# Kernel tuning notes

Hardware: AMD Instinct MI355X
Metric: run time of the kernel (lower is better)

The kernel has to match this reference:

```python
import jax, jax.numpy as jnp
import numpy as np

FACTOR = 5

def setup_inputs() -> dict:
    key = jax.random.key(0)
    kq, kk, kv, ki = jax.random.split(key, 4)
    B, L, H, D = 4, 4096, 8, 64
    sample_k = min(int(FACTOR * np.ceil(np.log(L))), L)  # 45
    queries = jax.random.normal(kq, (B, L, H, D), dtype=jnp.float32)
    keys = jax.random.normal(kk, (B, L, H, D), dtype=jnp.float32)
    values = jax.random.normal(kv, (B, L, H, D), dtype=jnp.float32)
    index_sample = jax.random.randint(ki, (L, sample_k), 0, L, dtype=jnp.int64)
    return {"queries": queries, "keys": keys, "values": values, "index_sample": index_sample}


def reference(queries, keys, values, index_sample):
    # queries/keys/values: (B, L, H, D); mask_flag=False, output_attention=False
    B, L_Q, H, D = queries.shape
    L_K = keys.shape[1]
    n_top = min(int(FACTOR * np.ceil(np.log(L_Q))), L_Q)
    scale = 1.0 / np.sqrt(D)

    Q = jnp.transpose(queries, (0, 2, 1, 3))  # (B,H,L_Q,D)
    K = jnp.transpose(keys, (0, 2, 1, 3))     # (B,H,L_K,D)
    V = jnp.transpose(values, (0, 2, 1, 3))   # (B,H,L_V,D)

    # --- _prob_QK: sample keys per query, score sparsity, keep top queries ---
    K_sample = K[:, :, index_sample, :]                       # (B,H,L_Q,S,D)
    Q_K_sample = jnp.einsum('bhqd,bhqsd->bhqs', Q, K_sample)  # (B,H,L_Q,S)
    M = Q_K_sample.max(axis=-1) - Q_K_sample.mean(axis=-1)    # (B,H,L_Q)
    _, M_top = jax.lax.top_k(M, n_top)                        # (B,H,n_top)
    Q_reduce = jnp.take_along_axis(Q, M_top[..., None], axis=2)  # (B,H,n_top,D)
    scores = jnp.einsum('bhnd,bhkd->bhnk', Q_reduce, K) * scale # (B,H,n_top,L_K)

    # --- initial context (mask_flag=False): mean of V over keys ---
    context = jnp.broadcast_to(V.mean(axis=2, keepdims=True), (B, H, L_Q, D))

    # --- update context at selected query positions ---
    attn = jax.nn.softmax(scores, axis=-1)                    # (B,H,n_top,L_K)
    upd = jnp.einsum('bhnk,bhkd->bhnd', attn, V)              # (B,H,n_top,D)
    bi = jnp.arange(B)[:, None, None]
    hi = jnp.arange(H)[None, :, None]
    context = context.at[bi, hi, M_top].set(upd)
    return context
```

## Files before the change

### kernel.cpp

```cpp
#include <hip/hip_runtime.h>
#include <math.h>

#define B_   4
#define L_   4096
#define H_   8
#define D_   64
#define SK   45
#define NT   45
#define BH   (B_*H_)
#define SCALE 0.125f
#define KC   256
#define JC2  16
#define VCH  64

typedef float vfloat4 __attribute__((ext_vector_type(4)));

__global__ __launch_bounds__(256) void k_m(const float* __restrict__ q,
                                           const float* __restrict__ k,
                                           const int* __restrict__ samp,
                                           float* __restrict__ M) {
  __shared__ int sid[8 * SK];
  const int ib   = blockIdx.x;
  const int x    = ib & 7;
  const int b    = x >> 1;
  const int half = x & 1;
  const int qi_base = (ib >> 3) * 8;
  const int tid = threadIdx.x;
  for (int i = tid; i < 8 * SK; i += 256)
    sid[i] = samp[(size_t)qi_base * SK + i];
  __syncthreads();

  const int w    = tid >> 6;
  const int lane = tid & 63;
  const int g2   = lane >> 5;
  const int l32  = lane & 31;
  const int hg   = l32 >> 3;
  const int r8   = l32 & 7;
  const int qi   = qi_base + w * 2 + g2;
  const int wq   = w * 2 + g2;

  const float* qbase = q + (((size_t)b * L_ + qi) * H_ + half * 4 + hg) * D_ + r8 * 8;
  const vfloat4 qa = __builtin_nontemporal_load((const vfloat4*)qbase);
  const vfloat4 qb4 = __builtin_nontemporal_load((const vfloat4*)(qbase + 4));

  const int* myids = sid + wq * SK;
  const float* kb2 = k + (size_t)b * L_ * (H_ * D_) + (half * 4 + hg) * D_ + r8 * 8;

  float gmax = -1e30f, gsum = 0.f;
  #pragma unroll 5
  for (int s = 0; s < SK; ++s) {
    const int id = myids[s];
    const float* kr = kb2 + (size_t)id * (H_ * D_);
    const vfloat4 ka  = *(const vfloat4*)kr;
    const vfloat4 kbv = *(const vfloat4*)(kr + 4);
    float p = qa.x*ka.x + qa.y*ka.y + qa.z*ka.z + qa.w*ka.w
            + qb4.x*kbv.x + qb4.y*kbv.y + qb4.z*kbv.z + qb4.w*kbv.w;
    { int t = __builtin_amdgcn_mov_dpp(__float_as_int(p), 0xB1, 0xf, 0xf, true); p += __int_as_float(t); }
    { int t = __builtin_amdgcn_mov_dpp(__float_as_int(p), 0x4E, 0xf, 0xf, true); p += __int_as_float(t); }
    { int t = __builtin_amdgcn_mov_dpp(__float_as_int(p), 0x141, 0xf, 0xf, true); p += __int_as_float(t); }
    gmax = fmaxf(gmax, p);
    gsum += p;
  }
  if (r8 == 0) M[((size_t)b * 8 + half * 4 + hg) * L_ + qi] = gmax - gsum * (1.0f / SK);
}

__global__ __launch_bounds__(256) void k_topk(const float* __restrict__ M,
                                              int* __restrict__ top) {
  __shared__ unsigned keys[L_];
  __shared__ unsigned hist[256];
  __shared__ unsigned wsum[4];
  __shared__ int sByte;
  __shared__ unsigned sAbove;
  __shared__ int cnt;
  const int bh = blockIdx.x, tid = threadIdx.x;
  const float* Mrow = M + (size_t)bh * L_;
  for (int i = tid; i < L_; i += 256) {
    const unsigned u = __float_as_uint(Mrow[i]);
    keys[i] = (u & 0x80000000u) ? ~u : (u | 0x80000000u);
  }
  unsigned prefix = 0u, fixed = 0u;
  unsigned remaining = NT;
  for (int p = 3; p >= 0; --p) {
    hist[tid] = 0u;
    __syncthreads();
    const int sh = p * 8;
    for (int i = tid; i < L_; i += 256) {
      const unsigned kk = keys[i];
      if ((kk & fixed) == prefix) atomicAdd(&hist[(kk >> sh) & 0xFFu], 1u);
    }
    __syncthreads();
    const int c = 255 - tid;
    const unsigned v = hist[c];
    unsigned x = v;
    #pragma unroll
    for (int o = 1; o < 64; o <<= 1) {
      const unsigned y = __shfl_up(x, o);
      if ((tid & 63) >= o) x += y;
    }
    if ((tid & 63) == 63) wsum[tid >> 6] = x;
    __syncthreads();
    unsigned off = 0;
    for (int w2 = 0; w2 < (tid >> 6); ++w2) off += wsum[w2];
    const unsigned Sincl = x + off;
    const unsigned Sab   = Sincl - v;
    if (Sab < remaining && remaining <= Sincl) { sByte = c; sAbove = Sab; }
    __syncthreads();
    prefix |= (unsigned)sByte << sh;
    fixed  |= 0xFFu << sh;
    remaining -= sAbove;
    __syncthreads();
  }
  if (tid == 0) cnt = 0;
  __syncthreads();
  int* trow = top + bh * NT;
  for (int i = tid; i < L_; i += 256) {
    if (keys[i] > prefix) { const int s = atomicAdd(&cnt, 1); trow[s] = i; }
  }
  __syncthreads();
  const int ngt = cnt;
  const int base = tid * 16;
  int lc = 0;
  #pragma unroll
  for (int j = 0; j < 16; ++j) lc += (keys[base + j] == prefix);
  unsigned x2 = (unsigned)lc;
  #pragma unroll
  for (int o = 1; o < 64; o <<= 1) {
    const unsigned y = __shfl_up(x2, o);
    if ((tid & 63) >= o) x2 += y;
  }
  if ((tid & 63) == 63) wsum[tid >> 6] = x2;
  __syncthreads();
  unsigned off2 = 0;
  for (int w2 = 0; w2 < (tid >> 6); ++w2) off2 += wsum[w2];
  unsigned rk = (x2 - (unsigned)lc) + off2;
  #pragma unroll
  for (int j = 0; j < 16; ++j) {
    if (keys[base + j] == prefix) {
      if (rk < remaining) trow[ngt + (int)rk] = base + j;
      ++rk;
    }
  }
}

__global__ __launch_bounds__(256) void k_vmean1(const float* __restrict__ v,
                                                float* __restrict__ vpart) {
  const int blk = blockIdx.x;
  const int b   = blk >> 6;
  const int c   = blk & 63;
  const int t   = threadIdx.x;
  const int hd4 = t & 127;
  const int p   = t >> 7;
  const float4* base = (const float4*)(v + ((size_t)b * L_ + (size_t)c * VCH) * (H_ * D_)) + hd4;
  float4 acc = {0.f, 0.f, 0.f, 0.f};
  for (int l = p; l < VCH; l += 2) {
    const float4 x = base[(size_t)l * 128];
    acc.x += x.x; acc.y += x.y; acc.z += x.z; acc.w += x.w;
  }
  __shared__ float4 s[2][128];
  s[p][hd4] = acc;
  __syncthreads();
  if (t < 128) {
    const float4 a = s[0][t], b2 = s[1][t];
    const float4 r = {a.x + b2.x, a.y + b2.y, a.z + b2.z, a.w + b2.w};
    ((float4*)vpart)[(size_t)blk * 128 + t] = r;
  }
}

__global__ __launch_bounds__(512) void k_vmean2(const float* __restrict__ vpart,
                                                float* __restrict__ vmean) {
  const int b = blockIdx.x, t = threadIdx.x;
  float acc = 0.f;
  for (int c = 0; c < 64; ++c)
    acc += vpart[((size_t)(b * 64 + c)) * 512 + t];
  vmean[b * 512 + t] = acc * (1.0f / L_);
}

__global__ __launch_bounds__(512) void k_attn(const float* __restrict__ q,
                                              const float* __restrict__ k,
                                              const float* __restrict__ v,
                                              const int* __restrict__ top,
                                              float* __restrict__ ml,
                                              float* __restrict__ opart) {
  __shared__ float lds_p[NT * 260];
  __shared__ __align__(16) float lds_q[NT * 64];
  __shared__ float lds_ml[NT * 2];
  const int bh = blockIdx.x >> 4, jc = blockIdx.x & 15;
  const int b = bh >> 3, h = bh & 7;
  const int tid = threadIdx.x;

  for (int fi = tid; fi < NT * 64; fi += 512) {
    const int n = fi >> 6, d = fi & 63;
    const int qi = top[bh * NT + n];
    lds_q[fi] = q[(((size_t)b * L_ + qi) * H_ + h) * D_ + d];
  }
  __syncthreads();

  {
    const int j = tid >> 1, dh = tid & 1;
    const float* krow_g = k + (((size_t)b * L_ + jc * KC + j) * H_ + h) * D_ + dh * 32;
    float kr[32];
    #pragma unroll
    for (int t4 = 0; t4 < 8; ++t4) {
      const vfloat4 kv = *(const vfloat4*)(krow_g + t4 * 4);
      kr[t4*4+0] = kv.x; kr[t4*4+1] = kv.y; kr[t4*4+2] = kv.z; kr[t4*4+3] = kv.w;
    }
    for (int n = 0; n < NT; ++n) {
      const float* qrow = &lds_q[n * 64 + dh * 32];
      float s = 0.f;
      #pragma unroll
      for (int t4 = 0; t4 < 8; ++t4) {
        const float4 qq = *(const float4*)(qrow + t4 * 4);
        s += qq.x*kr[t4*4] + qq.y*kr[t4*4+1] + qq.z*kr[t4*4+2] + qq.w*kr[t4*4+3];
      }
      { int t = __builtin_amdgcn_mov_dpp(__float_as_int(s), 0xB1, 0xf, 0xf, true); s += __int_as_float(t); }
      if (dh == 0) lds_p[n * 260 + j] = s * SCALE;
    }
  }
  __syncthreads();

  const int w = tid >> 6, lane = tid & 63;
  for (int n = w; n < NT; n += 8) {
    float* pr = &lds_p[n * 260];
    const float s0 = pr[lane], s1 = pr[64 + lane], s2 = pr[128 + lane], s3 = pr[192 + lane];
    float m = fmaxf(fmaxf(s0, s1), fmaxf(s2, s3));
    #pragma unroll
    for (int o = 1; o < 64; o <<= 1) m = fmaxf(m, __shfl_xor(m, o));
    const float p0 = __expf(s0 - m), p1 = __expf(s1 - m), p2 = __expf(s2 - m), p3 = __expf(s3 - m);
    float lsum = p0 + p1 + p2 + p3;
    #pragma unroll
    for (int o = 1; o < 64; o <<= 1) lsum += __shfl_xor(lsum, o);
    pr[lane] = p0; pr[64 + lane] = p1; pr[128 + lane] = p2; pr[192 + lane] = p3;
    if (lane == 0) { lds_ml[n * 2] = m; lds_ml[n * 2 + 1] = lsum; }
  }
  __syncthreads();

  const int d = lane;
  const int nn = (w < 5) ? 6 : 5;
  float acc[6];
  #pragma unroll
  for (int t = 0; t < 6; ++t) acc[t] = 0.f;
  const float* vbase = v + (((size_t)b * L_ + jc * KC) * H_ + h) * D_ + d;
  for (int j4 = 0; j4 < KC; j4 += 4) {
    float vv[4];
    #pragma unroll
    for (int u = 0; u < 4; ++u) vv[u] = vbase[(size_t)(j4 + u) * (H_ * D_)];
    #pragma unroll
    for (int t = 0; t < 6; ++t) {
      if (t < nn) {
        const int n = w + 8 * t;
        const float4 pv = *(const float4*)&lds_p[n * 260 + j4];
        acc[t] += pv.x * vv[0] + pv.y * vv[1] + pv.z * vv[2] + pv.w * vv[3];
      }
    }
  }
  float* obase = opart + (((size_t)bh * JC2 + jc) * NT) * 64;
  #pragma unroll
  for (int t = 0; t < 6; ++t)
    if (t < nn) obase[(w + 8 * t) * 64 + d] = acc[t];
  for (int i = tid; i < NT * 2; i += 512)
    ml[((size_t)bh * JC2 + jc) * (NT * 2) + i] = lds_ml[i];
}

__global__ __launch_bounds__(256) void k_fill(const float* __restrict__ vmean,
                                              float* __restrict__ out) {
  const size_t i = (size_t)blockIdx.x * 256 + threadIdx.x;
  const int d4 = (int)(i & 15);
  const int bh = (int)(i >> 16);
  const float4* vm = (const float4*)(vmean + bh * D_);
  ((float4*)out)[i] = vm[d4];
}

__global__ void k_comb(const float* __restrict__ opart,
                       const float* __restrict__ ml,
                       const int* __restrict__ top,
                       float* __restrict__ out) {
  const int bhn = blockIdx.x, bh = bhn / NT, n = bhn % NT;
  const int d = threadIdx.x;
  float mc[JC2], lc[JC2];
  float mg = -1e30f;
  #pragma unroll
  for (int c = 0; c < JC2; ++c) {
    mc[c] = ml[((size_t)bh * JC2 + c) * (NT * 2) + n * 2];
    lc[c] = ml[((size_t)bh * JC2 + c) * (NT * 2) + n * 2 + 1];
    mg = fmaxf(mg, mc[c]);
  }
  float den = 0.f, num = 0.f;
  #pragma unroll
  for (int c = 0; c < JC2; ++c) {
    const float wgt = __expf(mc[c] - mg);
    den += wgt * lc[c];
    num += wgt * opart[(((size_t)bh * JC2 + c) * NT + n) * 64 + d];
  }
  const int qi = top[bh * NT + n];
  out[((size_t)bh * L_ + qi) * 64 + d] = num / den;
}

extern "C" void kernel_launch(void* const* d_in, const int* in_sizes, int n_in,
                              void* d_out, int out_size, void* d_ws, size_t ws_size,
                              hipStream_t stream) {
  const float* q    = (const float*)d_in[0];
  const float* k    = (const float*)d_in[1];
  const float* v    = (const float*)d_in[2];
  const int*   samp = (const int*)d_in[3];
  float* out = (float*)d_out;
  char*  ws  = (char*)d_ws;

  float* M     = (float*)ws;
  int*   top   = (int*)(ws + 524288);
  float* vmean = (float*)(ws + 532480);
  float* opart = (float*)(ws + 540672);
  float* vpart = M;
  float* ml    = M;

  hipLaunchKernelGGL(k_m,      dim3(BH * L_ / 32), dim3(256), 0, stream, q, k, samp, M);
  hipLaunchKernelGGL(k_topk,   dim3(BH),           dim3(256), 0, stream, M, top);
  hipLaunchKernelGGL(k_vmean1, dim3(B_ * 64),      dim3(256), 0, stream, v, vpart);
  hipLaunchKernelGGL(k_vmean2, dim3(B_),           dim3(512), 0, stream, vpart, vmean);
  hipLaunchKernelGGL(k_attn,   dim3(BH * JC2),     dim3(512), 0, stream, q, k, v, top, ml, opart);
  hipLaunchKernelGGL(k_fill,   dim3(8192),         dim3(256), 0, stream, vmean, out);
  hipLaunchKernelGGL(k_comb,   dim3(BH * NT),      dim3(64),  0, stream, opart, ml, top, out);
}
```

Baseline: 156.6 us.

## Merge independent kernels via block-index dispatch and raise wave priority in attention loops

Merges seven launches into four by giving independent jobs their own block ranges. M-scoring runs alongside the V partial sums, top-k alongside the V-mean reduction, and attention alongside the mean fill of the output. This cuts launch gaps and lets small kernels share the GPU. The V partials move into the opart workspace so they do not clash with M. It also wraps the QK and PV loops in s_setprio to favour compute waves, at the cost of larger merged kernels whose LDS and register budget is set by the heaviest branch.

```diff
diff --git a/kernel.cpp b/kernel.cpp
--- a/kernel.cpp
+++ b/kernel.cpp
@@ -15,64 +15,101 @@
 
 typedef float vfloat4 __attribute__((ext_vector_type(4)));
 
-__global__ __launch_bounds__(256) void k_m(const float* __restrict__ q,
-                                           const float* __restrict__ k,
-                                           const int* __restrict__ samp,
-                                           float* __restrict__ M) {
-  __shared__ int sid[8 * SK];
-  const int ib   = blockIdx.x;
-  const int x    = ib & 7;
-  const int b    = x >> 1;
-  const int half = x & 1;
-  const int qi_base = (ib >> 3) * 8;
+__global__ __launch_bounds__(256) void k_mv(const float* __restrict__ q,
+                                            const float* __restrict__ k,
+                                            const int* __restrict__ samp,
+                                            const float* __restrict__ v,
+                                            float* __restrict__ M,
+                                            float* __restrict__ vpart) {
   const int tid = threadIdx.x;
-  for (int i = tid; i < 8 * SK; i += 256)
-    sid[i] = samp[(size_t)qi_base * SK + i];
-  __syncthreads();
-
-  const int w    = tid >> 6;
-  const int lane = tid & 63;
-  const int g2   = lane >> 5;
-  const int l32  = lane & 31;
-  const int hg   = l32 >> 3;
-  const int r8   = l32 & 7;
-  const int qi   = qi_base + w * 2 + g2;
-  const int wq   = w * 2 + g2;
-
-  const float* qbase = q + (((size_t)b * L_ + qi) * H_ + half * 4 + hg) * D_ + r8 * 8;
-  const vfloat4 qa = __builtin_nontemporal_load((const vfloat4*)qbase);
-  const vfloat4 qb4 = __builtin_nontemporal_load((const vfloat4*)(qbase + 4));
-
-  const int* myids = sid + wq * SK;
-  const float* kb2 = k + (size_t)b * L_ * (H_ * D_) + (half * 4 + hg) * D_ + r8 * 8;
-
-  float gmax = -1e30f, gsum = 0.f;
-  #pragma unroll 5
-  for (int s = 0; s < SK; ++s) {
-    const int id = myids[s];
-    const float* kr = kb2 + (size_t)id * (H_ * D_);
-    const vfloat4 ka  = *(const vfloat4*)kr;
-    const vfloat4 kbv = *(const vfloat4*)(kr + 4);
-    float p = qa.x*ka.x + qa.y*ka.y + qa.z*ka.z + qa.w*ka.w
-            + qb4.x*kbv.x + qb4.y*kbv.y + qb4.z*kbv.z + qb4.w*kbv.w;
-    { int t = __builtin_amdgcn_mov_dpp(__float_as_int(p), 0xB1, 0xf, 0xf, true); p += __int_as_float(t); }
-    { int t = __builtin_amdgcn_mov_dpp(__float_as_int(p), 0x4E, 0xf, 0xf, true); p += __int_as_float(t); }
-    { int t = __builtin_amdgcn_mov_dpp(__float_as_int(p), 0x141, 0xf, 0xf, true); p += __int_as_float(t); }
-    gmax = fmaxf(gmax, p);
-    gsum += p;
-  }
-  if (r8 == 0) M[((size_t)b * 8 + half * 4 + hg) * L_ + qi] = gmax - gsum * (1.0f / SK);
-}
-
-__global__ __launch_bounds__(256) void k_topk(const float* __restrict__ M,
-                                              int* __restrict__ top) {
+  if (blockIdx.x < 4096) {
+    __shared__ int sid[8 * SK];
+    const int ib   = blockIdx.x;
+    const int x    = ib & 7;
+    const int b    = x >> 1;
+    const int half = x & 1;
+    const int qi_base = (ib >> 3) * 8;
+    for (int i = tid; i < 8 * SK; i += 256)
+      sid[i] = samp[(size_t)qi_base * SK + i];
+    __syncthreads();
+
+    const int w    = tid >> 6;
+    const int lane = tid & 63;
+    const int g2   = lane >> 5;
+    const int l32  = lane & 31;
+    const int hg   = l32 >> 3;
+    const int r8   = l32 & 7;
+    const int qi   = qi_base + w * 2 + g2;
+    const int wq   = w * 2 + g2;
+
+    const float* qbase = q + (((size_t)b * L_ + qi) * H_ + half * 4 + hg) * D_ + r8 * 8;
+    const vfloat4 qa = __builtin_nontemporal_load((const vfloat4*)qbase);
+    const vfloat4 qb4 = __builtin_nontemporal_load((const vfloat4*)(qbase + 4));
+
+    const int* myids = sid + wq * SK;
+    const float* kb2 = k + (size_t)b * L_ * (H_ * D_) + (half * 4 + hg) * D_ + r8 * 8;
+
+    float gmax = -1e30f, gsum = 0.f;
+    #pragma unroll 5
+    for (int s = 0; s < SK; ++s) {
+      const int id = myids[s];
+      const float* kr = kb2 + (size_t)id * (H_ * D_);
+      const vfloat4 ka  = *(const vfloat4*)kr;
+      const vfloat4 kbv = *(const vfloat4*)(kr + 4);
+      float p = qa.x*ka.x + qa.y*ka.y + qa.z*ka.z + qa.w*ka.w
+              + qb4.x*kbv.x + qb4.y*kbv.y + qb4.z*kbv.z + qb4.w*kbv.w;
+      { int t = __builtin_amdgcn_mov_dpp(__float_as_int(p), 0xB1, 0xf, 0xf, true); p += __int_as_float(t); }
+      { int t = __builtin_amdgcn_mov_dpp(__float_as_int(p), 0x4E, 0xf, 0xf, true); p += __int_as_float(t); }
+      { int t = __builtin_amdgcn_mov_dpp(__float_as_int(p), 0x141, 0xf, 0xf, true); p += __int_as_float(t); }
+      gmax = fmaxf(gmax, p);
+      gsum += p;
+    }
+    if (r8 == 0) M[((size_t)b * 8 + half * 4 + hg) * L_ + qi] = gmax - gsum * (1.0f / SK);
+  } else {
+    const int blk = blockIdx.x - 4096;
+    const int b   = blk >> 6;
+    const int c   = blk & 63;
+    const int hd4 = tid & 127;
+    const int p   = tid >> 7;
+    const float4* base = (const float4*)(v + ((size_t)b * L_ + (size_t)c * VCH) * (H_ * D_)) + hd4;
+    float4 acc = {0.f, 0.f, 0.f, 0.f};
+    for (int l = p; l < VCH; l += 2) {
+      const float4 xv = base[(size_t)l * 128];
+      acc.x += xv.x; acc.y += xv.y; acc.z += xv.z; acc.w += xv.w;
+    }
+    __shared__ float4 s[2][128];
+    s[p][hd4] = acc;
+    __syncthreads();
+    if (tid < 128) {
+      const float4 a = s[0][tid], b2 = s[1][tid];
+      const float4 r = {a.x + b2.x, a.y + b2.y, a.z + b2.z, a.w + b2.w};
+      ((float4*)vpart)[(size_t)blk * 128 + tid] = r;
+    }
+  }
+}
+
+__global__ __launch_bounds__(256) void k_topkv(const float* __restrict__ M,
+                                               int* __restrict__ top,
+                                               const float* __restrict__ vpart,
+                                               float* __restrict__ vmean) {
+  const int tid = threadIdx.x;
+  if (blockIdx.x >= 32) {
+    const int b = blockIdx.x - 32;
+    for (int t = tid; t < 512; t += 256) {
+      float acc = 0.f;
+      for (int c = 0; c < 64; ++c)
+        acc += vpart[((size_t)(b * 64 + c)) * 512 + t];
+      vmean[b * 512 + t] = acc * (1.0f / L_);
+    }
+    return;
+  }
   __shared__ unsigned keys[L_];
   __shared__ unsigned hist[256];
   __shared__ unsigned wsum[4];
   __shared__ int sByte;
   __shared__ unsigned sAbove;
   __shared__ int cnt;
-  const int bh = blockIdx.x, tid = threadIdx.x;
+  const int bh = blockIdx.x;
   const float* Mrow = M + (size_t)bh * L_;
   for (int i = tid; i < L_; i += 256) {
     const unsigned u = __float_as_uint(Mrow[i]);
@@ -142,51 +179,28 @@
   }
 }
 
-__global__ __launch_bounds__(256) void k_vmean1(const float* __restrict__ v,
-                                                float* __restrict__ vpart) {
-  const int blk = blockIdx.x;
-  const int b   = blk >> 6;
-  const int c   = blk & 63;
-  const int t   = threadIdx.x;
-  const int hd4 = t & 127;
-  const int p   = t >> 7;
-  const float4* base = (const float4*)(v + ((size_t)b * L_ + (size_t)c * VCH) * (H_ * D_)) + hd4;
-  float4 acc = {0.f, 0.f, 0.f, 0.f};
-  for (int l = p; l < VCH; l += 2) {
-    const float4 x = base[(size_t)l * 128];
-    acc.x += x.x; acc.y += x.y; acc.z += x.z; acc.w += x.w;
-  }
-  __shared__ float4 s[2][128];
-  s[p][hd4] = acc;
-  __syncthreads();
-  if (t < 128) {
-    const float4 a = s[0][t], b2 = s[1][t];
-    const float4 r = {a.x + b2.x, a.y + b2.y, a.z + b2.z, a.w + b2.w};
-    ((float4*)vpart)[(size_t)blk * 128 + t] = r;
-  }
-}
-
-__global__ __launch_bounds__(512) void k_vmean2(const float* __restrict__ vpart,
-                                                float* __restrict__ vmean) {
-  const int b = blockIdx.x, t = threadIdx.x;
-  float acc = 0.f;
-  for (int c = 0; c < 64; ++c)
-    acc += vpart[((size_t)(b * 64 + c)) * 512 + t];
-  vmean[b * 512 + t] = acc * (1.0f / L_);
-}
-
-__global__ __launch_bounds__(512) void k_attn(const float* __restrict__ q,
-                                              const float* __restrict__ k,
-                                              const float* __restrict__ v,
-                                              const int* __restrict__ top,
-                                              float* __restrict__ ml,
-                                              float* __restrict__ opart) {
+__global__ __launch_bounds__(512) void k_attnf(const float* __restrict__ q,
+                                               const float* __restrict__ k,
+                                               const float* __restrict__ v,
+                                               const int* __restrict__ top,
+                                               const float* __restrict__ vmean,
+                                               float* __restrict__ ml,
+                                               float* __restrict__ opart,
+                                               float* __restrict__ out) {
   __shared__ float lds_p[NT * 260];
   __shared__ __align__(16) float lds_q[NT * 64];
   __shared__ float lds_ml[NT * 2];
+  const int tid = threadIdx.x;
+  if (blockIdx.x >= 512) {
+    const size_t i = (size_t)(blockIdx.x - 512) * 512 + tid;
+    const int d4 = (int)(i & 15);
+    const int bh = (int)(i >> 16);
+    const float4* vm = (const float4*)(vmean + bh * D_);
+    ((float4*)out)[i] = vm[d4];
+    return;
+  }
   const int bh = blockIdx.x >> 4, jc = blockIdx.x & 15;
   const int b = bh >> 3, h = bh & 7;
-  const int tid = threadIdx.x;
 
   for (int fi = tid; fi < NT * 64; fi += 512) {
     const int n = fi >> 6, d = fi & 63;
@@ -204,6 +218,7 @@
       const vfloat4 kv = *(const vfloat4*)(krow_g + t4 * 4);
       kr[t4*4+0] = kv.x; kr[t4*4+1] = kv.y; kr[t4*4+2] = kv.z; kr[t4*4+3] = kv.w;
     }
+    __builtin_amdgcn_s_setprio(1);
     for (int n = 0; n < NT; ++n) {
       const float* qrow = &lds_q[n * 64 + dh * 32];
       float s = 0.f;
@@ -215,6 +230,7 @@
       { int t = __builtin_amdgcn_mov_dpp(__float_as_int(s), 0xB1, 0xf, 0xf, true); s += __int_as_float(t); }
       if (dh == 0) lds_p[n * 260 + j] = s * SCALE;
     }
+    __builtin_amdgcn_s_setprio(0);
   }
   __syncthreads();
 
@@ -240,6 +256,7 @@
   #pragma unroll
   for (int t = 0; t < 6; ++t) acc[t] = 0.f;
   const float* vbase = v + (((size_t)b * L_ + jc * KC) * H_ + h) * D_ + d;
+  __builtin_amdgcn_s_setprio(1);
   for (int j4 = 0; j4 < KC; j4 += 4) {
     float vv[4];
     #pragma unroll
@@ -253,21 +270,13 @@
       }
     }
   }
+  __builtin_amdgcn_s_setprio(0);
   float* obase = opart + (((size_t)bh * JC2 + jc) * NT) * 64;
   #pragma unroll
   for (int t = 0; t < 6; ++t)
     if (t < nn) obase[(w + 8 * t) * 64 + d] = acc[t];
   for (int i = tid; i < NT * 2; i += 512)
     ml[((size_t)bh * JC2 + jc) * (NT * 2) + i] = lds_ml[i];
-}
-
-__global__ __launch_bounds__(256) void k_fill(const float* __restrict__ vmean,
-                                              float* __restrict__ out) {
-  const size_t i = (size_t)blockIdx.x * 256 + threadIdx.x;
-  const int d4 = (int)(i & 15);
-  const int bh = (int)(i >> 16);
-  const float4* vm = (const float4*)(vmean + bh * D_);
-  ((float4*)out)[i] = vm[d4];
 }
 
 __global__ void k_comb(const float* __restrict__ opart,
@@ -309,14 +318,11 @@
   int*   top   = (int*)(ws + 524288);
   float* vmean = (float*)(ws + 532480);
   float* opart = (float*)(ws + 540672);
-  float* vpart = M;
+  float* vpart = opart;
   float* ml    = M;
 
-  hipLaunchKernelGGL(k_m,      dim3(BH * L_ / 32), dim3(256), 0, stream, q, k, samp, M);
-  hipLaunchKernelGGL(k_topk,   dim3(BH),           dim3(256), 0, stream, M, top);
-  hipLaunchKernelGGL(k_vmean1, dim3(B_ * 64),      dim3(256), 0, stream, v, vpart);
-  hipLaunchKernelGGL(k_vmean2, dim3(B_),           dim3(512), 0, stream, vpart, vmean);
-  hipLaunchKernelGGL(k_attn,   dim3(BH * JC2),     dim3(512), 0, stream, q, k, v, top, ml, opart);
-  hipLaunchKernelGGL(k_fill,   dim3(8192),         dim3(256), 0, stream, vmean, out);
-  hipLaunchKernelGGL(k_comb,   dim3(BH * NT),      dim3(64),  0, stream, opart, ml, top, out);
-}
+  hipLaunchKernelGGL(k_mv,    dim3(4096 + 256),  dim3(256), 0, stream, q, k, samp, v, M, vpart);
+  hipLaunchKernelGGL(k_topkv, dim3(36),          dim3(256), 0, stream, M, top, vpart, vmean);
+  hipLaunchKernelGGL(k_attnf, dim3(512 + 4096),  dim3(512), 0, stream, q, k, v, top, vmean, ml, opart, out);
+  hipLaunchKernelGGL(k_comb,  dim3(BH * NT),     dim3(64),  0, stream, opart, ml, top, out);
+}
```

After: 145.6 us, median of 2. -7.1%, faster.
